# Kernel tuning notes

Measured on AMD Instinct MI355X. Metric: run time of the kernel, lower is better.

Reference implementation:

```python
import jax, jax.numpy as jnp
import numpy as np

B = 2; R_PER = 512; R = B * R_PER; RM_PER = 128; RM = B * RM_PER
NUM_CLASSES = 81; C = 256
IMG_H = 800.0; IMG_W = 800.0
SCALES = (0.25, 0.125, 0.0625, 0.03125)  # FPN strides 4,8,16,32
REG_W = (10.0, 10.0, 5.0, 5.0)
LOG_1000_16 = 4.135166556742356  # math.log(1000/16)


def _prep(c, size):
    # torchvision roi_align (aligned=False) coordinate handling
    valid = (c > -1.0) & (c < size)
    c = jnp.clip(c, 0.0, size - 1.0)
    lo = jnp.clip(jnp.floor(c), 0.0, size - 2.0).astype(jnp.int32)
    frac = c - lo.astype(c.dtype)
    return lo, frac, valid


def roi_align(feat, boxes, b_idx, scale, out_size, sr=2):
    # feat [B,C,H,W], boxes [R,4] in image coords, b_idx [R] int
    _, Cn, H, W = feat.shape
    bb = boxes * scale
    x1, y1 = bb[:, 0], bb[:, 1]
    rw = jnp.maximum(bb[:, 2] - x1, 1.0)
    rh = jnp.maximum(bb[:, 3] - y1, 1.0)
    n = out_size * sr
    g = (jnp.arange(n, dtype=feat.dtype) + 0.5) / (sr * out_size)
    ys = y1[:, None] + rh[:, None] * g[None, :]  # [R,n]
    xs = x1[:, None] + rw[:, None] * g[None, :]
    y0, ly, yv = _prep(ys, H)
    x0, lx, xv = _prep(xs, W)
    bi = b_idx[:, None, None]
    yy = y0[:, :, None]; xx = x0[:, None, :]
    f00 = feat[bi, :, yy, xx]          # [R,n,n,C]
    f01 = feat[bi, :, yy, xx + 1]
    f10 = feat[bi, :, yy + 1, xx]
    f11 = feat[bi, :, yy + 1, xx + 1]
    ly_ = ly[:, :, None, None]; lx_ = lx[:, None, :, None]
    v = (f00 * (1 - ly_) * (1 - lx_) + f01 * (1 - ly_) * lx_
         + f10 * ly_ * (1 - lx_) + f11 * ly_ * lx_)
    mask = (yv[:, :, None] & xv[:, None, :]).astype(v.dtype)[..., None]
    v = v * mask
    Rn = boxes.shape[0]
    v = v.reshape(Rn, out_size, sr, out_size, sr, Cn).mean(axis=(2, 4))
    return jnp.transpose(v, (0, 3, 1, 2))  # [R,C,out,out]


def multiscale_roi_align(feats, boxes, b_idx, out_size):
    area = jnp.maximum(boxes[:, 2] - boxes[:, 0], 0.0) * jnp.maximum(boxes[:, 3] - boxes[:, 1], 0.0)
    lvl = jnp.clip(jnp.floor(4.0 + jnp.log2(jnp.sqrt(area) / 224.0 + 1e-6)), 2.0, 5.0).astype(jnp.int32) - 2
    out = 0.0
    for i, (f, s) in enumerate(zip(feats, SCALES)):
        out = out + roi_align(f, boxes, b_idx, s, out_size) * (lvl == i)[:, None, None, None].astype(f.dtype)
    return out


def decode_boxes(deltas, boxes):
    # deltas [R,K,4], boxes [R,4]
    wx, wy, ww, wh = REG_W
    w = boxes[:, 2] - boxes[:, 0]; h = boxes[:, 3] - boxes[:, 1]
    cx = boxes[:, 0] + 0.5 * w; cy = boxes[:, 1] + 0.5 * h
    dx = deltas[..., 0] / wx; dy = deltas[..., 1] / wy
    dw = jnp.minimum(deltas[..., 2] / ww, LOG_1000_16)
    dh = jnp.minimum(deltas[..., 3] / wh, LOG_1000_16)
    pcx = dx * w[:, None] + cx[:, None]; pcy = dy * h[:, None] + cy[:, None]
    pw = jnp.exp(dw) * w[:, None]; ph = jnp.exp(dh) * h[:, None]
    out = jnp.stack([pcx - 0.5 * pw, pcy - 0.5 * ph, pcx + 0.5 * pw, pcy + 0.5 * ph], axis=-1)
    hi = jnp.array([IMG_W, IMG_H, IMG_W, IMG_H], dtype=out.dtype)
    return jnp.clip(out, 0.0, hi)  # process_box clip-to-image


def conv3x3(x, w, b):
    y = jax.lax.conv_general_dilated(x, w, (1, 1), ((1, 1), (1, 1)),
                                     dimension_numbers=('NCHW', 'OIHW', 'NCHW'))
    return jax.nn.relu(y + b[None, :, None, None])


def _forward(feat0, feat1, feat2, feat3, proposals, fc1_w, fc1_b, fc2_w, fc2_b,
             cls_w, cls_b, bbox_w, bbox_b, mconv_w, mconv_b, deconv_w, deconv_b,
             mlogit_w, mlogit_b, batch_idx):
    feats = (feat0, feat1, feat2, feat3)
    # box branch
    bf = multiscale_roi_align(feats, proposals, batch_idx, 7).reshape(R, -1)  # [R, 256*49]
    x = jax.nn.relu(bf @ fc1_w.T + fc1_b)
    x = jax.nn.relu(x @ fc2_w.T + fc2_b)
    scores = jax.nn.softmax(x @ cls_w.T + cls_b, axis=-1)          # [R,81]
    deltas = (x @ bbox_w.T + bbox_b).reshape(R, NUM_CLASSES, 4)
    boxes = decode_boxes(deltas, proposals)                        # [R,81,4]
    # mask branch on top-of-list detections (RM_PER per image), box at argmax fg class
    idx_m = jnp.concatenate([jnp.arange(RM_PER), R_PER + jnp.arange(RM_PER)])
    labels = jnp.argmax(scores[idx_m, 1:], axis=-1) + 1            # [RM]
    mboxes = boxes[idx_m, labels]                                  # [RM,4]
    mf = multiscale_roi_align(feats, mboxes, batch_idx[idx_m], 14)  # [RM,256,14,14]
    for i in range(4):
        mf = conv3x3(mf, mconv_w[i], mconv_b[i])
    # ConvTranspose2d k=2 s=2 (non-overlapping) as einsum, PyTorch IOHW weights
    t = jnp.einsum('bcij,copq->boipjq', mf, deconv_w).reshape(RM, C, 28, 28)
    t = jax.nn.relu(t + deconv_b[None, :, None, None])
    ml = jnp.einsum('bchw,oc->bohw', t, mlogit_w) + mlogit_b[None, :, None, None]
    masks = jax.nn.sigmoid(ml[jnp.arange(RM), labels])             # [RM,28,28]
    return scores, boxes, masks


def setup_inputs() -> dict:
    key = jax.random.key(0)
    ks = jax.random.split(key, 16)
    rn = lambda i, shape, s=1.0: jax.random.normal(ks[i], shape, dtype=jnp.float32) * s
    feat0 = rn(0, (B, C, 200, 200))
    feat1 = rn(1, (B, C, 100, 100))
    feat2 = rn(2, (B, C, 50, 50))
    feat3 = rn(3, (B, C, 25, 25))
    u = jax.random.uniform(ks[4], (R, 4), dtype=jnp.float32)
    x1 = u[:, 0] * (IMG_W - 64.0); y1 = u[:, 1] * (IMG_H - 64.0)
    w = 16.0 + u[:, 2] * 300.0; h = 16.0 + u[:, 3] * 300.0
    proposals = jnp.stack([x1, y1, jnp.minimum(x1 + w, IMG_W), jnp.minimum(y1 + h, IMG_H)], axis=1)
    batch_idx = jnp.repeat(jnp.arange(B, dtype=jnp.int32), R_PER)
    return dict(
        feat0=feat0, feat1=feat1, feat2=feat2, feat3=feat3,
        proposals=proposals,
        fc1_w=rn(5, (1024, C * 49), 0.01), fc1_b=jnp.zeros(1024, jnp.float32),
        fc2_w=rn(6, (1024, 1024), 0.02), fc2_b=jnp.zeros(1024, jnp.float32),
        cls_w=rn(7, (NUM_CLASSES, 1024), 0.02), cls_b=jnp.zeros(NUM_CLASSES, jnp.float32),
        bbox_w=rn(8, (NUM_CLASSES * 4, 1024), 0.01), bbox_b=jnp.zeros(NUM_CLASSES * 4, jnp.float32),
        mconv_w=rn(9, (4, C, C, 3, 3), 0.03), mconv_b=jnp.zeros((4, C), jnp.float32),
        deconv_w=rn(10, (C, C, 2, 2), 0.06), deconv_b=jnp.zeros(C, jnp.float32),
        mlogit_w=rn(11, (NUM_CLASSES, C), 0.06), mlogit_b=jnp.zeros(NUM_CLASSES, jnp.float32),
        batch_idx=batch_idx,
    )


def reference(feat0, feat1, feat2, feat3, proposals, fc1_w, fc1_b, fc2_w, fc2_b,
              cls_w, cls_b, bbox_w, bbox_b, mconv_w, mconv_b, deconv_w, deconv_b,
              mlogit_w, mlogit_b, batch_idx):
    return _forward(feat0, feat1, feat2, feat3, proposals, fc1_w, fc1_b, fc2_w, fc2_b,
                    cls_w, cls_b, bbox_w, bbox_b, mconv_w, mconv_b, deconv_w, deconv_b,
                    mlogit_w, mlogit_b, batch_idx)
```

## Files before the change

kernel.cpp:

```cpp
#include <hip/hip_runtime.h>


#define NUM_CLASSES 81
#define CDIM 256
#define RTOT 1024
#define RMASK 256
#define LOG1000_16 4.135166556742356f

typedef _Float16 half8v __attribute__((ext_vector_type(8)));
typedef _Float16 half4v __attribute__((ext_vector_type(4)));
typedef float    float4v __attribute__((ext_vector_type(4)));
typedef float    float2a4 __attribute__((ext_vector_type(2), aligned(4)));

__device__ __forceinline__ void gload_lds16(const void* g, void* l) {
    __builtin_amdgcn_global_load_lds(
        (const __attribute__((address_space(1))) void*)g,
        (__attribute__((address_space(3))) void*)l, 16, 0, 0);
}

__global__ __launch_bounds__(256) void roi_align7_kernel(
    const float* __restrict__ f0, const float* __restrict__ f1,
    const float* __restrict__ f2, const float* __restrict__ f3,
    const float* __restrict__ props, const int* __restrict__ bidx,
    _Float16* __restrict__ bf_h, _Float16* __restrict__ bf_l)
{
    int r  = blockIdx.x;
    int cg = blockIdx.y;
    int t = threadIdx.x;
    if (t >= 196) return;
    int p  = t % 49;
    int cl = t / 49;
    int oy = p / 7, ox = p % 7;

    float x1 = props[r*4+0], y1 = props[r*4+1];
    float x2 = props[r*4+2], y2 = props[r*4+3];
    float area = fmaxf(x2-x1, 0.f) * fmaxf(y2-y1, 0.f);
    float lf = floorf(4.f + log2f(sqrtf(area)/224.f + 1e-6f));
    lf = fminf(fmaxf(lf, 2.f), 5.f);
    int lvl = (int)lf - 2;

    const float* feat; int H, W; float scale;
    if (lvl == 0)      { feat = f0; H = 200; W = 200; scale = 0.25f; }
    else if (lvl == 1) { feat = f1; H = 100; W = 100; scale = 0.125f; }
    else if (lvl == 2) { feat = f2; H = 50;  W = 50;  scale = 0.0625f; }
    else               { feat = f3; H = 25;  W = 25;  scale = 0.03125f; }
    int b = bidx[r];

    float x1s = x1*scale, y1s = y1*scale;
    float rw = fmaxf(x2*scale - x1s, 1.f);
    float rh = fmaxf(y2*scale - y1s, 1.f);

    int   offs[4];
    float w00[4], w01[4], w10[4], w11[4];
    #pragma unroll
    for (int sy = 0; sy < 2; ++sy) {
        int iy = oy*2 + sy;
        float gy = ((float)iy + 0.5f) / 14.f;
        float yc = y1s + rh*gy;
        bool  yv = (yc > -1.f) && (yc < (float)H);
        float ycl = fminf(fmaxf(yc, 0.f), (float)(H-1));
        int   y0  = (int)fminf(floorf(ycl), (float)(H-2));
        float ly  = ycl - (float)y0;
        #pragma unroll
        for (int sx = 0; sx < 2; ++sx) {
            int ix = ox*2 + sx;
            float gx = ((float)ix + 0.5f) / 14.f;
            float xc = x1s + rw*gx;
            bool  xv = (xc > -1.f) && (xc < (float)W);
            float xcl = fminf(fmaxf(xc, 0.f), (float)(W-1));
            int   x0  = (int)fminf(floorf(xcl), (float)(W-2));
            float lx  = xcl - (float)x0;
            float m = (yv && xv) ? 1.f : 0.f;
            int s = sy*2 + sx;
            offs[s] = y0*W + x0;
            w00[s] = (1.f-ly)*(1.f-lx)*m;
            w01[s] = (1.f-ly)*lx*m;
            w10[s] = ly*(1.f-lx)*m;
            w11[s] = ly*lx*m;
        }
    }

    size_t HW = (size_t)H * W;
    #pragma unroll 4
    for (int k = 0; k < 16; ++k) {
        int c = cg*64 + cl + k*4;
        const float* fb = feat + ((size_t)b*CDIM + c) * HW;
        float acc = 0.f;
        #pragma unroll
        for (int s = 0; s < 4; ++s) {
            const float* q = fb + offs[s];
            float2a4 u = *(const float2a4*)q;
            float2a4 v = *(const float2a4*)(q + W);
            acc += w00[s]*u.x + w01[s]*u.y + w10[s]*v.x + w11[s]*v.y;
        }
        float v = acc * 0.25f;
        _Float16 h = (_Float16)v;
        size_t o = (size_t)r*12544 + c*49 + p;
        bf_h[o] = h;
        bf_l[o] = (_Float16)((v - (float)h) * 2048.f);
    }
}

template<bool BSPLIT>
__global__ __launch_bounds__(256, 2) void gemm_fc(
    const _Float16* __restrict__ Ah, const _Float16* __restrict__ Al,
    const float* __restrict__ B32,
    const _Float16* __restrict__ Bh16, const _Float16* __restrict__ Bl16,
    float* __restrict__ Cp, int K, int KS, int NS)
{
    __shared__ _Float16 AhL[2][128*32];
    __shared__ _Float16 AlL[2][128*32];
    __shared__ _Float16 BhL[2][64*32];
    __shared__ _Float16 BlL[2][64*32];

    int t = threadIdx.x;
    int lane = t & 63, wave = t >> 6;
    int wm = wave >> 1, wn = wave & 1;
    int ln = lane & 15, q = lane >> 4;

    int gx = gridDim.x, gy = gridDim.y;
    int lin = blockIdx.x + gx*(blockIdx.y + gy*blockIdx.z);
    int per = (gx*gy*(int)gridDim.z) >> 3;
    int nl  = (lin & 7)*per + (lin >> 3);
    int bn  = nl % gx;
    int tmp = nl / gx;
    int bm  = tmp % gy;
    int kz  = tmp / gy;

    int asub = lane >> 2;
    int achk = (lane & 3) ^ ((lane >> 3) & 3);
    int arow0 = (wave*2+0)*16 + asub;
    int arow1 = (wave*2+1)*16 + asub;
    const _Float16* Agh0 = Ah + (size_t)(bm*128+arow0)*K + (size_t)kz*KS + achk*8;
    const _Float16* Agh1 = Ah + (size_t)(bm*128+arow1)*K + (size_t)kz*KS + achk*8;
    const _Float16* Agl0 = Al + (size_t)(bm*128+arow0)*K + (size_t)kz*KS + achk*8;
    const _Float16* Agl1 = Al + (size_t)(bm*128+arow1)*K + (size_t)kz*KS + achk*8;
    int adst0 = (wave*2+0)*512;
    int adst1 = (wave*2+1)*512;

    const float*    Bs32 = nullptr;
    const _Float16 *Bgh = nullptr, *Bgl = nullptr;
    int bdst = 0, bwoff = 0;
    if constexpr (BSPLIT) {
        int brow = wave*16 + asub;
        Bgh = Bh16 + (size_t)(bn*64+brow)*K + (size_t)kz*KS + achk*8;
        Bgl = Bl16 + (size_t)(bn*64+brow)*K + (size_t)kz*KS + achk*8;
        bdst = wave*512;
    } else {
        int brow = t >> 2, bcp = t & 3;
        int bch = bcp ^ ((brow >> 1) & 3);
        Bs32 = B32 + (size_t)(bn*64+brow)*K + (size_t)kz*KS + bcp*8;
        bwoff = brow*32 + bch*8;
    }

    float4v acc1[4][2], acc2[4][2];
    #pragma unroll
    for (int i = 0; i < 4; ++i)
        #pragma unroll
        for (int j = 0; j < 2; ++j) {
            acc1[i][j] = (float4v){0.f,0.f,0.f,0.f};
            acc2[i][j] = (float4v){0.f,0.f,0.f,0.f};
        }

    int cq = (q ^ ((ln >> 1) & 3)) * 8;

    auto dma = [&](int k0, int nb) {
        gload_lds16(Agh0 + k0, &AhL[nb][adst0]);
        gload_lds16(Agh1 + k0, &AhL[nb][adst1]);
        gload_lds16(Agl0 + k0, &AlL[nb][adst0]);
        gload_lds16(Agl1 + k0, &AlL[nb][adst1]);
        if constexpr (BSPLIT) {
            gload_lds16(Bgh + k0, &BhL[nb][bdst]);
            gload_lds16(Bgl + k0, &BlL[nb][bdst]);
        }
    };
    auto bwrite = [&](const float4& v0, const float4& v1, int nb) {
        float vv[8] = {v0.x,v0.y,v0.z,v0.w,v1.x,v1.y,v1.z,v1.w};
        half8v h, l;
        #pragma unroll
        for (int j = 0; j < 8; ++j) {
            _Float16 hj = (_Float16)vv[j];
            h[j] = hj;
            l[j] = (_Float16)((vv[j] - (float)hj) * 2048.f);
        }
        *(half8v*)&BhL[nb][bwoff] = h;
        *(half8v*)&BlL[nb][bwoff] = l;
    };
    auto compute = [&](int pb) {
        half8v afh[4], afl[4], bfh[2], bfl[2];
        #pragma unroll
        for (int i = 0; i < 4; ++i) {
            int ra = (wm*64 + i*16 + ln)*32 + cq;
            afh[i] = *(const half8v*)&AhL[pb][ra];
            afl[i] = *(const half8v*)&AlL[pb][ra];
        }
        #pragma unroll
        for (int j = 0; j < 2; ++j) {
            int rb = (wn*32 + j*16 + ln)*32 + cq;
            bfh[j] = *(const half8v*)&BhL[pb][rb];
            bfl[j] = *(const half8v*)&BlL[pb][rb];
        }
        #pragma unroll
        for (int i = 0; i < 4; ++i) {
            #pragma unroll
            for (int j = 0; j < 2; ++j) {
                acc1[i][j] = __builtin_amdgcn_mfma_f32_16x16x32_f16(
                    afh[i], bfh[j], acc1[i][j], 0, 0, 0);
                acc2[i][j] = __builtin_amdgcn_mfma_f32_16x16x32_f16(
                    afh[i], bfl[j], acc2[i][j], 0, 0, 0);
                acc2[i][j] = __builtin_amdgcn_mfma_f32_16x16x32_f16(
                    afl[i], bfh[j], acc2[i][j], 0, 0, 0);
            }
        }
    };

    float4 bv0, bv1;
    if constexpr (!BSPLIT) {
        bv0 = *(const float4*)(Bs32);
        bv1 = *(const float4*)(Bs32 + 4);
    }
    dma(0, 0);
    if constexpr (!BSPLIT) bwrite(bv0, bv1, 0);
    __syncthreads();

    int pb = 0;
    for (int k0 = 32; k0 < KS; k0 += 32) {
        if constexpr (!BSPLIT) {
            bv0 = *(const float4*)(Bs32 + k0);
            bv1 = *(const float4*)(Bs32 + k0 + 4);
        }
        dma(k0, pb ^ 1);
        compute(pb);
        if constexpr (!BSPLIT) bwrite(bv0, bv1, pb ^ 1);
        __syncthreads();
        pb ^= 1;
    }
    compute(pb);

    float* Cpz = Cp + (size_t)kz*1024*NS;
    #pragma unroll
    for (int i = 0; i < 4; ++i) {
        #pragma unroll
        for (int j = 0; j < 2; ++j) {
            int col = bn*64 + wn*32 + j*16 + ln;
            #pragma unroll
            for (int reg = 0; reg < 4; ++reg) {
                int row = bm*128 + wm*64 + i*16 + q*4 + reg;
                Cpz[(size_t)row*NS + col] =
                    acc1[i][j][reg] + acc2[i][j][reg] * (1.f/2048.f);
            }
        }
    }
}

__global__ __launch_bounds__(256) void fc_reduce_kernel(
    const float* __restrict__ Cp, const float* __restrict__ bias,
    float* __restrict__ out, _Float16* __restrict__ outh,
    _Float16* __restrict__ outl, int nparts, int ns4, int do_relu)
{
    int i = blockIdx.x*256 + threadIdx.x;
    const float4* p = (const float4*)Cp;
    int pstride = 1024*ns4;
    float sx = 0.f, sy = 0.f, sz = 0.f, sw = 0.f;
    for (int j = 0; j < nparts; ++j) {
        float4 s = p[i + j*pstride];
        sx += s.x; sy += s.y; sz += s.z; sw += s.w;
    }
    float4 b4 = ((const float4*)bias)[i & (ns4-1)];
    float4 v;
    v.x = sx + b4.x; v.y = sy + b4.y; v.z = sz + b4.z; v.w = sw + b4.w;
    if (do_relu) {
        v.x = fmaxf(v.x, 0.f); v.y = fmaxf(v.y, 0.f);
        v.z = fmaxf(v.z, 0.f); v.w = fmaxf(v.w, 0.f);
    }
    if (out) ((float4*)out)[i] = v;
    if (outh) {
        float vv[4] = {v.x, v.y, v.z, v.w};
        half4v hh, hl;
        #pragma unroll
        for (int c2 = 0; c2 < 4; ++c2) {
            _Float16 h = (_Float16)vv[c2];
            hh[c2] = h;
            hl[c2] = (_Float16)((vv[c2] - (float)h) * 2048.f);
        }
        ((half4v*)outh)[i] = hh;
        ((half4v*)outl)[i] = hl;
    }
}

__global__ __launch_bounds__(256) void repack_head_kernel(
    const float* __restrict__ cls_w, const float* __restrict__ cls_b,
    const float* __restrict__ bbox_w, const float* __restrict__ bbox_b,
    _Float16* __restrict__ Wcat_h, _Float16* __restrict__ Wcat_l,
    float* __restrict__ bcat)
{
    int i = blockIdx.x*256 + threadIdx.x;
    int row = i >> 10, col = i & 1023;
    float v = 0.f;
    if (row < 81) v = cls_w[row*1024 + col];
    else if (row < 405) v = bbox_w[(row-81)*1024 + col];
    _Float16 h = (_Float16)v;
    Wcat_h[i] = h;
    Wcat_l[i] = (_Float16)((v - (float)h) * 2048.f);
    if (i < 512) {
        float bv = 0.f;
        if (i < 81) bv = cls_b[i];
        else if (i < 405) bv = bbox_b[i-81];
        bcat[i] = bv;
    }
}

__global__ __launch_bounds__(128) void heads_finish_kernel(
    const float* __restrict__ L, const float* __restrict__ props,
    float* __restrict__ scores, float* __restrict__ boxes,
    int* __restrict__ labels, float* __restrict__ mboxes)
{
    __shared__ float lg[NUM_CLASSES];
    __shared__ float red[2];
    __shared__ int slab;
    int r = blockIdx.x, t = threadIdx.x;
    const float* Lr = L + (size_t)r*512;
    if (t < NUM_CLASSES) lg[t] = Lr[t];
    __syncthreads();
    if (t == 0) {
        float mx = lg[0];
        for (int j = 1; j < NUM_CLASSES; ++j) mx = fmaxf(mx, lg[j]);
        red[0] = mx;
    }
    __syncthreads();
    float mx = red[0];
    if (t < NUM_CLASSES) lg[t] = expf(lg[t] - mx);
    __syncthreads();
    if (t == 0) {
        float s = 0.f;
        int best = 1; float bv = lg[1];
        for (int j = 0; j < NUM_CLASSES; ++j) {
            s += lg[j];
            if (j >= 1 && lg[j] > bv) { bv = lg[j]; best = j; }
        }
        red[1] = 1.f/s;
        slab = best;
    }
    __syncthreads();
    if (t < NUM_CLASSES) scores[(size_t)r*NUM_CLASSES + t] = lg[t]*red[1];

    bool sel = (r < 128) || (r >= 512 && r < 640);
    int mi = (r < 128) ? r : r - 384;
    if (t == 0 && sel) labels[mi] = slab;

    if (t < NUM_CLASSES) {
        float px1 = props[r*4+0], py1 = props[r*4+1];
        float px2 = props[r*4+2], py2 = props[r*4+3];
        float pw = px2 - px1, ph = py2 - py1;
        float cx = px1 + 0.5f*pw, cy = py1 + 0.5f*ph;
        const float* dl = Lr + 81 + t*4;
        float d0 = dl[0] * 0.1f;
        float d1 = dl[1] * 0.1f;
        float d2 = fminf(dl[2] * 0.2f, LOG1000_16);
        float d3 = fminf(dl[3] * 0.2f, LOG1000_16);
        float pcx = d0*pw + cx, pcy = d1*ph + cy;
        float qw = expf(d2)*pw, qh = expf(d3)*ph;
        float b0 = fminf(fmaxf(pcx - 0.5f*qw, 0.f), 800.f);
        float b1 = fminf(fmaxf(pcy - 0.5f*qh, 0.f), 800.f);
        float b2 = fminf(fmaxf(pcx + 0.5f*qw, 0.f), 800.f);
        float b3 = fminf(fmaxf(pcy + 0.5f*qh, 0.f), 800.f);
        size_t ob = ((size_t)r*NUM_CLASSES + t)*4;
        boxes[ob+0] = b0; boxes[ob+1] = b1; boxes[ob+2] = b2; boxes[ob+3] = b3;
        if (sel && t == slab) {
            mboxes[mi*4+0] = b0; mboxes[mi*4+1] = b1;
            mboxes[mi*4+2] = b2; mboxes[mi*4+3] = b3;
        }
    }
}

__global__ __launch_bounds__(256) void roi_align14_kernel(
    const float* __restrict__ f0, const float* __restrict__ f1,
    const float* __restrict__ f2, const float* __restrict__ f3,
    const float* __restrict__ mboxes, const int* __restrict__ bidx,
    _Float16* __restrict__ outT)
{
    int mi = blockIdx.x;
    int cg = blockIdx.y;
    int t = threadIdx.x;
    if (t >= 196) return;
    int oy = t / 14, ox = t % 14;

    float x1 = mboxes[mi*4+0], y1 = mboxes[mi*4+1];
    float x2 = mboxes[mi*4+2], y2 = mboxes[mi*4+3];
    float area = fmaxf(x2-x1, 0.f) * fmaxf(y2-y1, 0.f);
    float lf = floorf(4.f + log2f(sqrtf(area)/224.f + 1e-6f));
    lf = fminf(fmaxf(lf, 2.f), 5.f);
    int lvl = (int)lf - 2;

    const float* feat; int H, W; float scale;
    if (lvl == 0)      { feat = f0; H = 200; W = 200; scale = 0.25f; }
    else if (lvl == 1) { feat = f1; H = 100; W = 100; scale = 0.125f; }
    else if (lvl == 2) { feat = f2; H = 50;  W = 50;  scale = 0.0625f; }
    else               { feat = f3; H = 25;  W = 25;  scale = 0.03125f; }
    int ridx = (mi < 128) ? mi : mi + 384;
    int b = bidx[ridx];

    float x1s = x1*scale, y1s = y1*scale;
    float rw = fmaxf(x2*scale - x1s, 1.f);
    float rh = fmaxf(y2*scale - y1s, 1.f);

    int   offs[4];
    float w00[4], w01[4], w10[4], w11[4];
    #pragma unroll
    for (int sy = 0; sy < 2; ++sy) {
        int iy = oy*2 + sy;
        float gy = ((float)iy + 0.5f) / 28.f;
        float yc = y1s + rh*gy;
        bool  yv = (yc > -1.f) && (yc < (float)H);
        float ycl = fminf(fmaxf(yc, 0.f), (float)(H-1));
        int   y0  = (int)fminf(floorf(ycl), (float)(H-2));
        float ly  = ycl - (float)y0;
        #pragma unroll
        for (int sx = 0; sx < 2; ++sx) {
            int ix = ox*2 + sx;
            float gx = ((float)ix + 0.5f) / 28.f;
            float xc = x1s + rw*gx;
            bool  xv = (xc > -1.f) && (xc < (float)W);
            float xcl = fminf(fmaxf(xc, 0.f), (float)(W-1));
            int   x0  = (int)fminf(floorf(xcl), (float)(W-2));
            float lx  = xcl - (float)x0;
            float m = (yv && xv) ? 1.f : 0.f;
            int s = sy*2 + sx;
            offs[s] = y0*W + x0;
            w00[s] = (1.f-ly)*(1.f-lx)*m;
            w01[s] = (1.f-ly)*lx*m;
            w10[s] = ly*(1.f-lx)*m;
            w11[s] = ly*lx*m;
        }
    }

    size_t HW = (size_t)H * W;
    _Float16* orow = outT + ((size_t)mi*196 + t)*CDIM + cg*32;
    const float* fbase = feat + ((size_t)b*CDIM + cg*32) * HW;
    #pragma unroll
    for (int c8 = 0; c8 < 32; c8 += 8) {
        half8v hv;
        #pragma unroll
        for (int cc = 0; cc < 8; ++cc) {
            const float* fb = fbase + (size_t)(c8+cc) * HW;
            float acc = 0.f;
            #pragma unroll
            for (int s = 0; s < 4; ++s) {
                const float* q = fb + offs[s];
                float2a4 u = *(const float2a4*)q;
                float2a4 v = *(const float2a4*)(q + W);
                acc += w00[s]*u.x + w01[s]*u.y + w10[s]*v.x + w11[s]*v.y;
            }
            hv[cc] = (_Float16)(acc * 0.25f);
        }
        *(half8v*)(orow + c8) = hv;
    }
}

__global__ __launch_bounds__(256) void repack_wts_kernel(
    const float* __restrict__ w, _Float16* __restrict__ Wr)
{
    int i = blockIdx.x*256 + threadIdx.x;
    int ci = i & 255;
    int rest = i >> 8;
    int co = rest & 255;
    int rest2 = rest >> 8;
    int tap = rest2 % 9;
    int l = rest2 / 9;
    Wr[i] = (_Float16)w[(((size_t)(l*256 + co)*256 + ci)*9) + tap];
}

__global__ __launch_bounds__(256) void repack_dw_kernel(
    const float* __restrict__ dw, _Float16* __restrict__ Wd)
{
    int i = blockIdx.x*256 + threadIdx.x;
    int n = i >> 8, k = i & 255;
    Wd[i] = (_Float16)dw[(size_t)k*1024 + n];
}

#define PSTR 40

__global__ __launch_bounds__(256, 2) void conv3x3_mfma_kernel(
    const _Float16* __restrict__ inT, const _Float16* __restrict__ Wr,
    const float* __restrict__ bias, _Float16* __restrict__ outT, int layer)
{
    __shared__ _Float16 lin[256*PSTR];

    int t = threadIdx.x;
    int lane = t & 63;
    int wave = t >> 6;
    int ln = lane & 15;
    int q  = lane >> 4;
    int q8 = q*8;
    int r  = blockIdx.x >> 1;
    int bc = blockIdx.x & 1;
    int co_w = bc*128 + wave*32;

    const _Float16* WrL = Wr + (size_t)layer*9*256*256;
    const _Float16* inR = inT + (size_t)r*196*256;

    for (int i = t; i < 256*PSTR; i += 256) lin[i] = (_Float16)0.f;

    float4v acc[13][2];
    #pragma unroll
    for (int nt = 0; nt < 13; ++nt) {
        acc[nt][0] = (float4v){0.f,0.f,0.f,0.f};
        acc[nt][1] = (float4v){0.f,0.f,0.f,0.f};
    }

    for (int ci0 = 0; ci0 < 256; ci0 += 32) {
        __syncthreads();
        for (int idx = t; idx < 784; idx += 256) {
            int p = idx >> 2, g = idx & 3;
            float4 v = *(const float4*)(inR + (size_t)p*256 + ci0 + g*8);
            int row = (p*37450) >> 19;
            int col = p - row*14;
            *(float4*)&lin[((row+1)*16 + (col+1))*PSTR + g*8] = v;
        }
        __syncthreads();

        half8v aw[9][2];
        #pragma unroll
        for (int tap = 0; tap < 9; ++tap) {
            #pragma unroll
            for (int u = 0; u < 2; ++u)
                aw[tap][u] = *(const half8v*)(
                    WrL + ((size_t)tap*256 + co_w + u*16 + ln)*256 + ci0 + q8);
        }

        #pragma unroll
        for (int nt = 0; nt < 13; ++nt) {
            int n = nt*16 + ln;
            int row = (n*37450) >> 19;
            int col = n - row*14;
            int pb = (n < 196) ? (row*16 + col) : 0;
            const _Float16* bp = &lin[pb*PSTR + q8];
            #pragma unroll
            for (int ky = 0; ky < 3; ++ky) {
                #pragma unroll
                for (int kx = 0; kx < 3; ++kx) {
                    half8v bv = *(const half8v*)(bp + (ky*16 + kx)*PSTR);
                    acc[nt][0] = __builtin_amdgcn_mfma_f32_16x16x32_f16(
                        aw[ky*3+kx][0], bv, acc[nt][0], 0, 0, 0);
                    acc[nt][1] = __builtin_amdgcn_mfma_f32_16x16x32_f16(
                        aw[ky*3+kx][1], bv, acc[nt][1], 0, 0, 0);
                }
            }
        }
    }

    #pragma unroll
    for (int u = 0; u < 2; ++u) {
        float4 bi = *(const float4*)&bias[layer*256 + co_w + u*16 + q*4];
        float bia[4] = {bi.x, bi.y, bi.z, bi.w};
        #pragma unroll
        for (int nt = 0; nt < 13; ++nt) {
            int n = nt*16 + ln;
            if (n < 196) {
                half4v hv;
                #pragma unroll
                for (int i = 0; i < 4; ++i)
                    hv[i] = (_Float16)fmaxf(acc[nt][u][i] + bia[i], 0.f);
                *(half4v*)(outT + ((size_t)r*196 + n)*256 + co_w + u*16 + q*4) = hv;
            }
        }
    }
}

#define DSTR 264

template<int NMT>
__device__ __forceinline__ void deconv_pass(
    const _Float16* actL, const _Float16* __restrict__ Wd,
    const float* __restrict__ db, const float* __restrict__ mlw,
    int lab, float (*sred)[4], int wv, int ln, int q, int px0)
{
    float P[NMT][4];
    #pragma unroll
    for (int mt = 0; mt < NMT; ++mt)
        #pragma unroll
        for (int r2 = 0; r2 < 4; ++r2) P[mt][r2] = 0.f;

    for (int c = 0; c < 8; ++c) {
        int n0 = wv*256 + c*32;
        float4v acc[NMT][2];
        #pragma unroll
        for (int mt = 0; mt < NMT; ++mt) {
            acc[mt][0] = (float4v){0.f,0.f,0.f,0.f};
            acc[mt][1] = (float4v){0.f,0.f,0.f,0.f};
        }
        #pragma unroll
        for (int k = 0; k < 8; ++k) {
            const _Float16* wp = Wd + ((size_t)(n0 + ln))*256 + k*32 + q*8;
            half8v b0 = *(const half8v*)wp;
            half8v b1 = *(const half8v*)(wp + 16*256);
            #pragma unroll
            for (int mt = 0; mt < NMT; ++mt) {
                half8v a = *(const half8v*)&actL[(mt*16 + ln)*DSTR + k*32 + q*8];
                acc[mt][0] = __builtin_amdgcn_mfma_f32_16x16x32_f16(
                    a, b0, acc[mt][0], 0, 0, 0);
                acc[mt][1] = __builtin_amdgcn_mfma_f32_16x16x32_f16(
                    a, b1, acc[mt][1], 0, 0, 0);
            }
        }
        #pragma unroll
        for (int j = 0; j < 2; ++j) {
            int n = n0 + j*16 + ln;
            int o = n >> 2;
            float bo = db[o];
            float wl = mlw[lab*256 + o];
            #pragma unroll
            for (int mt = 0; mt < NMT; ++mt)
                #pragma unroll
                for (int r2 = 0; r2 < 4; ++r2)
                    P[mt][r2] += fmaxf(acc[mt][j][r2] + bo, 0.f) * wl;
        }
    }
    #pragma unroll
    for (int mt = 0; mt < NMT; ++mt)
        #pragma unroll
        for (int r2 = 0; r2 < 4; ++r2) {
            float v = P[mt][r2];
            v += __shfl_xor(v, 4);
            v += __shfl_xor(v, 8);
            int px = px0 + mt*16 + q*4 + r2;
            if (ln < 4 && px < 196) atomicAdd(&sred[px][ln], v);
        }
}

__global__ __launch_bounds__(256, 1) void deconv_mask_mfma_kernel(
    const _Float16* __restrict__ mfT, const _Float16* __restrict__ Wd,
    const float* __restrict__ db, const float* __restrict__ mlw,
    const float* __restrict__ mlb, const int* __restrict__ labels,
    float* __restrict__ masks)
{
    __shared__ _Float16 act[112*DSTR];
    __shared__ float sred[196][4];
    int t = threadIdx.x;
    int lane = t & 63, wv = t >> 6, ln = lane & 15, q = lane >> 4;
    int mi = blockIdx.x;
    int lab = labels[mi];

    for (int i = t; i < 784; i += 256) ((float*)sred)[i] = 0.f;

    for (int idx = t; idx < 112*32; idx += 256) {
        int px = idx >> 5, g = idx & 31;
        *(float4*)&act[px*DSTR + g*8] =
            *(const float4*)(mfT + ((size_t)mi*196 + px)*256 + g*8);
    }
    __syncthreads();
    deconv_pass<7>(act, Wd, db, mlw, lab, sred, wv, ln, q, 0);
    __syncthreads();

    for (int idx = t; idx < 84*32; idx += 256) {
        int px = idx >> 5, g = idx & 31;
        *(float4*)&act[px*DSTR + g*8] =
            *(const float4*)(mfT + ((size_t)mi*196 + 112 + px)*256 + g*8);
    }
    __syncthreads();
    deconv_pass<6>(act, Wd, db, mlw, lab, sred, wv, ln, q, 112);
    __syncthreads();

    if (t < 196) {
        float bl = mlb[lab];
        int i2 = t / 14, j2 = t % 14;
        #pragma unroll
        for (int pq = 0; pq < 4; ++pq) {
            float s = sred[t][pq] + bl;
            int h = 2*i2 + (pq >> 1), w2 = 2*j2 + (pq & 1);
            masks[(size_t)mi*784 + h*28 + w2] = 1.f/(1.f + expf(-s));
        }
    }
}

extern "C" void kernel_launch(void* const* d_in, const int* in_sizes, int n_in,
                              void* d_out, int out_size, void* d_ws, size_t ws_size,
                              hipStream_t stream) {
    const float* f0      = (const float*)d_in[0];
    const float* f1      = (const float*)d_in[1];
    const float* f2      = (const float*)d_in[2];
    const float* f3      = (const float*)d_in[3];
    const float* props   = (const float*)d_in[4];
    const float* fc1_w   = (const float*)d_in[5];
    const float* fc1_b   = (const float*)d_in[6];
    const float* fc2_w   = (const float*)d_in[7];
    const float* fc2_b   = (const float*)d_in[8];
    const float* cls_w   = (const float*)d_in[9];
    const float* cls_b   = (const float*)d_in[10];
    const float* bbox_w  = (const float*)d_in[11];
    const float* bbox_b  = (const float*)d_in[12];
    const float* mconv_w = (const float*)d_in[13];
    const float* mconv_b = (const float*)d_in[14];
    const float* dconv_w = (const float*)d_in[15];
    const float* dconv_b = (const float*)d_in[16];
    const float* mlog_w  = (const float*)d_in[17];
    const float* mlog_b  = (const float*)d_in[18];
    const int*   bidx    = (const int*)d_in[19];

    char* wsb = (char*)d_ws;
    _Float16* bf_h = (_Float16*)wsb;
    _Float16* bf_l = (_Float16*)(wsb + 25690112);
    _Float16* bufA = (_Float16*)wsb;
    _Float16* bufB = (_Float16*)(wsb + 25690112);
    _Float16* x1h  = (_Float16*)(wsb + 51380224);
    _Float16* x1l  = (_Float16*)(wsb + 53477376);
    _Float16* x2h  = (_Float16*)(wsb + 55574528);
    _Float16* x2l  = (_Float16*)(wsb + 57671680);
    int*      labels = (int*)(wsb + 59768832);
    float*    mboxes = (float*)(wsb + 59772928);
    float*    Cp     = (float*)(wsb + 59781120);
    _Float16* Wr     = (_Float16*)(wsb + 59781120);
    _Float16* Wd     = (_Float16*)(wsb + 64499712);
    _Float16* Wcat_h = (_Float16*)(wsb + 76558336);
    _Float16* Wcat_l = (_Float16*)(wsb + 77606912);
    float*    bcat   = (float*)(wsb + 78655488);
    float*    Lh     = (float*)(wsb + 78659584);

    float* scores = (float*)d_out;
    float* boxes  = scores + RTOT*NUM_CLASSES;
    float* masks  = boxes + RTOT*NUM_CLASSES*4;

    roi_align7_kernel<<<dim3(RTOT, 4), 256, 0, stream>>>(
        f0, f1, f2, f3, props, bidx, bf_h, bf_l);

    repack_head_kernel<<<2048, 256, 0, stream>>>(cls_w, cls_b, bbox_w, bbox_b,
                                                 Wcat_h, Wcat_l, bcat);

    gemm_fc<false><<<dim3(16, 8, 4), 256, 0, stream>>>(
        bf_h, bf_l, fc1_w, nullptr, nullptr, Cp, 12544, 3136, 1024);
    fc_reduce_kernel<<<1024, 256, 0, stream>>>(Cp, fc1_b, nullptr, x1h, x1l,
                                               4, 256, 1);

    gemm_fc<false><<<dim3(16, 8, 4), 256, 0, stream>>>(
        x1h, x1l, fc2_w, nullptr, nullptr, Cp, 1024, 256, 1024);
    fc_reduce_kernel<<<1024, 256, 0, stream>>>(Cp, fc2_b, nullptr, x2h, x2l,
                                               4, 256, 1);

    gemm_fc<true><<<dim3(8, 8, 4), 256, 0, stream>>>(
        x2h, x2l, nullptr, Wcat_h, Wcat_l, Cp, 1024, 256, 512);
    fc_reduce_kernel<<<512, 256, 0, stream>>>(Cp, bcat, Lh, nullptr, nullptr,
                                              4, 128, 0);

    heads_finish_kernel<<<RTOT, 128, 0, stream>>>(Lh, props, scores, boxes,
                                                  labels, mboxes);

    repack_wts_kernel<<<4*9*256, 256, 0, stream>>>(mconv_w, Wr);
    repack_dw_kernel<<<1024, 256, 0, stream>>>(dconv_w, Wd);

    roi_align14_kernel<<<dim3(RMASK, 8), 256, 0, stream>>>(
        f0, f1, f2, f3, mboxes, bidx, bufA);

    conv3x3_mfma_kernel<<<RMASK*2, 256, 0, stream>>>(bufA, Wr, mconv_b, bufB, 0);
    conv3x3_mfma_kernel<<<RMASK*2, 256, 0, stream>>>(bufB, Wr, mconv_b, bufA, 1);
    conv3x3_mfma_kernel<<<RMASK*2, 256, 0, stream>>>(bufA, Wr, mconv_b, bufB, 2);
    conv3x3_mfma_kernel<<<RMASK*2, 256, 0, stream>>>(bufB, Wr, mconv_b, bufA, 3);

    deconv_mask_mfma_kernel<<<RMASK, 256, 0, stream>>>(bufA, Wd, dconv_b, mlog_w,
                                                       mlog_b, labels, masks);
}
```

Measured before the change: 926.9 us.

## Rework FC GEMMs: 128x128 tiles, triple-buffered LDS DMA, fp32 B via LDS

Replaces the FC GEMM kernel with a 128x128 tile version that uses a three-stage LDS ring filled by async global-to-LDS loads, with vmcnt waits and a single barrier per k-step. For fc1, the fp32 weights are DMA'd into LDS with an XOR swizzle and split into fp16 hi/lo at fragment-load time, instead of being loaded into registers and written back to LDS. fc2 weights are pre-split by a new repack kernel, and the head GEMM uses split-K 8. The goal is to cut global traffic for the large fc1 weight and hide load latency, at the cost of occupancy one, 96KB of LDS and more conversion work in the inner loop.

```diff
diff --git a/kernel.cpp b/kernel.cpp
--- a/kernel.cpp
+++ b/kernel.cpp
@@ -101,17 +101,14 @@
     }
 }
 
-template<bool BSPLIT>
-__global__ __launch_bounds__(256, 2) void gemm_fc(
+template<int BMODE>
+__global__ __launch_bounds__(256, 1) void gemm_fc2(
     const _Float16* __restrict__ Ah, const _Float16* __restrict__ Al,
     const float* __restrict__ B32,
     const _Float16* __restrict__ Bh16, const _Float16* __restrict__ Bl16,
     float* __restrict__ Cp, int K, int KS, int NS)
 {
-    __shared__ _Float16 AhL[2][128*32];
-    __shared__ _Float16 AlL[2][128*32];
-    __shared__ _Float16 BhL[2][64*32];
-    __shared__ _Float16 BlL[2][64*32];
+    __shared__ __align__(16) char smem[3*32768];
 
     int t = threadIdx.x;
     int lane = t & 63, wave = t >> 6;
@@ -127,83 +124,114 @@
     int bm  = tmp % gy;
     int kz  = tmp / gy;
 
+    size_t kbase = (size_t)kz * KS;
     int asub = lane >> 2;
     int achk = (lane & 3) ^ ((lane >> 3) & 3);
-    int arow0 = (wave*2+0)*16 + asub;
-    int arow1 = (wave*2+1)*16 + asub;
-    const _Float16* Agh0 = Ah + (size_t)(bm*128+arow0)*K + (size_t)kz*KS + achk*8;
-    const _Float16* Agh1 = Ah + (size_t)(bm*128+arow1)*K + (size_t)kz*KS + achk*8;
-    const _Float16* Agl0 = Al + (size_t)(bm*128+arow0)*K + (size_t)kz*KS + achk*8;
-    const _Float16* Agl1 = Al + (size_t)(bm*128+arow1)*K + (size_t)kz*KS + achk*8;
-    int adst0 = (wave*2+0)*512;
-    int adst1 = (wave*2+1)*512;
-
-    const float*    Bs32 = nullptr;
-    const _Float16 *Bgh = nullptr, *Bgl = nullptr;
-    int bdst = 0, bwoff = 0;
-    if constexpr (BSPLIT) {
-        int brow = wave*16 + asub;
-        Bgh = Bh16 + (size_t)(bn*64+brow)*K + (size_t)kz*KS + achk*8;
-        Bgl = Bl16 + (size_t)(bn*64+brow)*K + (size_t)kz*KS + achk*8;
-        bdst = wave*512;
+
+    const _Float16* Agh0 = Ah + (size_t)(bm*128 + wave*32 + asub)*K + kbase + achk*8;
+    const _Float16* Agh1 = Agh0 + (size_t)16*K;
+    const _Float16* Agl0 = Al + (size_t)(bm*128 + wave*32 + asub)*K + kbase + achk*8;
+    const _Float16* Agl1 = Agl0 + (size_t)16*K;
+    int adst0 = (wave*32 + 0)*32;
+    int adst1 = (wave*32 + 16)*32;
+
+    const _Float16 *Bgh0=nullptr, *Bgh1=nullptr, *Bgl0=nullptr, *Bgl1=nullptr;
+    const float *Bg0=nullptr, *Bg1=nullptr, *Bg2=nullptr, *Bg3=nullptr;
+    int fdst0 = 0;
+    if constexpr (BMODE == 1) {
+        Bgh0 = Bh16 + (size_t)(bn*128 + wave*32 + asub)*K + kbase + achk*8;
+        Bgh1 = Bgh0 + (size_t)16*K;
+        Bgl0 = Bl16 + (size_t)(bn*128 + wave*32 + asub)*K + kbase + achk*8;
+        Bgl1 = Bgl0 + (size_t)16*K;
     } else {
-        int brow = t >> 2, bcp = t & 3;
-        int bch = bcp ^ ((brow >> 1) & 3);
-        Bs32 = B32 + (size_t)(bn*64+brow)*K + (size_t)kz*KS + bcp*8;
-        bwoff = brow*32 + bch*8;
-    }
-
-    float4v acc1[4][2], acc2[4][2];
+        int br8  = lane >> 3;
+        int bchk = (lane & 7) ^ br8;
+        const float* base = B32 + (size_t)(bn*128 + wave*32 + br8)*K + kbase + bchk*4;
+        Bg0 = base;
+        Bg1 = base + (size_t)8*K;
+        Bg2 = base + (size_t)16*K;
+        Bg3 = base + (size_t)24*K;
+        fdst0 = (wave*32)*32;
+    }
+
+    auto AhB = [&](int b){ return (_Float16*)(smem + b*32768); };
+    auto AlB = [&](int b){ return (_Float16*)(smem + b*32768 + 8192); };
+    auto BhB = [&](int b){ return (_Float16*)(smem + b*32768 + 16384); };
+    auto BlB = [&](int b){ return (_Float16*)(smem + b*32768 + 24576); };
+    auto BfB = [&](int b){ return (float*)   (smem + b*32768 + 16384); };
+
+    auto dma = [&](int k0, int b) {
+        gload_lds16(Agh0 + k0, AhB(b) + adst0);
+        gload_lds16(Agh1 + k0, AhB(b) + adst1);
+        gload_lds16(Agl0 + k0, AlB(b) + adst0);
+        gload_lds16(Agl1 + k0, AlB(b) + adst1);
+        if constexpr (BMODE == 1) {
+            gload_lds16(Bgh0 + k0, BhB(b) + adst0);
+            gload_lds16(Bgh1 + k0, BhB(b) + adst1);
+            gload_lds16(Bgl0 + k0, BlB(b) + adst0);
+            gload_lds16(Bgl1 + k0, BlB(b) + adst1);
+        } else {
+            gload_lds16(Bg0 + k0, BfB(b) + fdst0);
+            gload_lds16(Bg1 + k0, BfB(b) + fdst0 + 8*32);
+            gload_lds16(Bg2 + k0, BfB(b) + fdst0 + 16*32);
+            gload_lds16(Bg3 + k0, BfB(b) + fdst0 + 24*32);
+        }
+    };
+
+    float4v acc1[4][4], acc2[4][4];
     #pragma unroll
     for (int i = 0; i < 4; ++i)
         #pragma unroll
-        for (int j = 0; j < 2; ++j) {
+        for (int j = 0; j < 4; ++j) {
             acc1[i][j] = (float4v){0.f,0.f,0.f,0.f};
             acc2[i][j] = (float4v){0.f,0.f,0.f,0.f};
         }
 
     int cq = (q ^ ((ln >> 1) & 3)) * 8;
 
-    auto dma = [&](int k0, int nb) {
-        gload_lds16(Agh0 + k0, &AhL[nb][adst0]);
-        gload_lds16(Agh1 + k0, &AhL[nb][adst1]);
-        gload_lds16(Agl0 + k0, &AlL[nb][adst0]);
-        gload_lds16(Agl1 + k0, &AlL[nb][adst1]);
-        if constexpr (BSPLIT) {
-            gload_lds16(Bgh + k0, &BhL[nb][bdst]);
-            gload_lds16(Bgl + k0, &BlL[nb][bdst]);
-        }
-    };
-    auto bwrite = [&](const float4& v0, const float4& v1, int nb) {
-        float vv[8] = {v0.x,v0.y,v0.z,v0.w,v1.x,v1.y,v1.z,v1.w};
-        half8v h, l;
-        #pragma unroll
-        for (int j = 0; j < 8; ++j) {
-            _Float16 hj = (_Float16)vv[j];
-            h[j] = hj;
-            l[j] = (_Float16)((vv[j] - (float)hj) * 2048.f);
-        }
-        *(half8v*)&BhL[nb][bwoff] = h;
-        *(half8v*)&BlL[nb][bwoff] = l;
-    };
-    auto compute = [&](int pb) {
-        half8v afh[4], afl[4], bfh[2], bfl[2];
+    auto compute = [&](int b) {
+        const _Float16* ah = AhB(b);
+        const _Float16* al = AlB(b);
+        half8v afh[4], afl[4], bfh[4], bfl[4];
         #pragma unroll
         for (int i = 0; i < 4; ++i) {
             int ra = (wm*64 + i*16 + ln)*32 + cq;
-            afh[i] = *(const half8v*)&AhL[pb][ra];
-            afl[i] = *(const half8v*)&AlL[pb][ra];
-        }
-        #pragma unroll
-        for (int j = 0; j < 2; ++j) {
-            int rb = (wn*32 + j*16 + ln)*32 + cq;
-            bfh[j] = *(const half8v*)&BhL[pb][rb];
-            bfl[j] = *(const half8v*)&BlL[pb][rb];
+            afh[i] = *(const half8v*)&ah[ra];
+            afl[i] = *(const half8v*)&al[ra];
+        }
+        if constexpr (BMODE == 1) {
+            const _Float16* bh = BhB(b);
+            const _Float16* bl = BlB(b);
+            #pragma unroll
+            for (int j = 0; j < 4; ++j) {
+                int rb = (wn*64 + j*16 + ln)*32 + cq;
+                bfh[j] = *(const half8v*)&bh[rb];
+                bfl[j] = *(const half8v*)&bl[rb];
+            }
+        } else {
+            const float* bfp = BfB(b);
+            #pragma unroll
+            for (int j = 0; j < 4; ++j) {
+                int row = wn*64 + j*16 + ln;
+                int c0 = (q*2)   ^ (row & 7);
+                int c1 = (q*2+1) ^ (row & 7);
+                float4v f0 = *(const float4v*)&bfp[row*32 + c0*4];
+                float4v f1 = *(const float4v*)&bfp[row*32 + c1*4];
+                #pragma unroll
+                for (int e = 0; e < 4; ++e) {
+                    _Float16 h0 = (_Float16)f0[e];
+                    bfh[j][e] = h0;
+                    bfl[j][e] = (_Float16)((f0[e] - (float)h0) * 2048.f);
+                    _Float16 h1 = (_Float16)f1[e];
+                    bfh[j][4+e] = h1;
+                    bfl[j][4+e] = (_Float16)((f1[e] - (float)h1) * 2048.f);
+                }
+            }
         }
         #pragma unroll
         for (int i = 0; i < 4; ++i) {
             #pragma unroll
-            for (int j = 0; j < 2; ++j) {
+            for (int j = 0; j < 4; ++j) {
                 acc1[i][j] = __builtin_amdgcn_mfma_f32_16x16x32_f16(
                     afh[i], bfh[j], acc1[i][j], 0, 0, 0);
                 acc2[i][j] = __builtin_amdgcn_mfma_f32_16x16x32_f16(
@@ -214,35 +242,25 @@
         }
     };
 
-    float4 bv0, bv1;
-    if constexpr (!BSPLIT) {
-        bv0 = *(const float4*)(Bs32);
-        bv1 = *(const float4*)(Bs32 + 4);
-    }
+    int NT = KS / 32;
     dma(0, 0);
-    if constexpr (!BSPLIT) bwrite(bv0, bv1, 0);
-    __syncthreads();
-
-    int pb = 0;
-    for (int k0 = 32; k0 < KS; k0 += 32) {
-        if constexpr (!BSPLIT) {
-            bv0 = *(const float4*)(Bs32 + k0);
-            bv1 = *(const float4*)(Bs32 + k0 + 4);
-        }
-        dma(k0, pb ^ 1);
-        compute(pb);
-        if constexpr (!BSPLIT) bwrite(bv0, bv1, pb ^ 1);
-        __syncthreads();
-        pb ^= 1;
-    }
-    compute(pb);
+    if (NT > 1) dma(32, 1);
+
+    for (int tt = 0; tt < NT; ++tt) {
+        if (tt < NT-1) asm volatile("s_waitcnt vmcnt(8)" ::: "memory");
+        else           asm volatile("s_waitcnt vmcnt(0)" ::: "memory");
+        __builtin_amdgcn_s_barrier();
+        asm volatile("" ::: "memory");
+        if (tt + 2 < NT) dma((tt+2)*32, (tt+2)%3);
+        compute(tt%3);
+    }
 
     float* Cpz = Cp + (size_t)kz*1024*NS;
     #pragma unroll
     for (int i = 0; i < 4; ++i) {
         #pragma unroll
-        for (int j = 0; j < 2; ++j) {
-            int col = bn*64 + wn*32 + j*16 + ln;
+        for (int j = 0; j < 4; ++j) {
+            int col = bn*128 + wn*64 + j*16 + ln;
             #pragma unroll
             for (int reg = 0; reg < 4; ++reg) {
                 int row = bm*128 + wm*64 + i*16 + q*4 + reg;
@@ -286,6 +304,24 @@
         ((half4v*)outh)[i] = hh;
         ((half4v*)outl)[i] = hl;
     }
+}
+
+__global__ __launch_bounds__(256) void repack_split_kernel(
+    const float* __restrict__ w, _Float16* __restrict__ h,
+    _Float16* __restrict__ l)
+{
+    int i = blockIdx.x*256 + threadIdx.x;
+    float4 v = ((const float4*)w)[i];
+    float vv[4] = {v.x, v.y, v.z, v.w};
+    half4v hh, hl;
+    #pragma unroll
+    for (int c2 = 0; c2 < 4; ++c2) {
+        _Float16 hj = (_Float16)vv[c2];
+        hh[c2] = hj;
+        hl[c2] = (_Float16)((vv[c2] - (float)hj) * 2048.f);
+    }
+    ((half4v*)h)[i] = hh;
+    ((half4v*)l)[i] = hl;
 }
 
 __global__ __launch_bounds__(256) void repack_head_kernel(
@@ -700,6 +736,8 @@
     char* wsb = (char*)d_ws;
     _Float16* bf_h = (_Float16*)wsb;
     _Float16* bf_l = (_Float16*)(wsb + 25690112);
+    _Float16* fc2h = (_Float16*)wsb;
+    _Float16* fc2l = (_Float16*)(wsb + 2097152);
     _Float16* bufA = (_Float16*)wsb;
     _Float16* bufB = (_Float16*)(wsb + 25690112);
     _Float16* x1h  = (_Float16*)(wsb + 51380224);
@@ -726,20 +764,22 @@
     repack_head_kernel<<<2048, 256, 0, stream>>>(cls_w, cls_b, bbox_w, bbox_b,
                                                  Wcat_h, Wcat_l, bcat);
 
-    gemm_fc<false><<<dim3(16, 8, 4), 256, 0, stream>>>(
+    gemm_fc2<0><<<dim3(8, 8, 4), 256, 0, stream>>>(
         bf_h, bf_l, fc1_w, nullptr, nullptr, Cp, 12544, 3136, 1024);
     fc_reduce_kernel<<<1024, 256, 0, stream>>>(Cp, fc1_b, nullptr, x1h, x1l,
                                                4, 256, 1);
 
-    gemm_fc<false><<<dim3(16, 8, 4), 256, 0, stream>>>(
-        x1h, x1l, fc2_w, nullptr, nullptr, Cp, 1024, 256, 1024);
+    repack_split_kernel<<<1024, 256, 0, stream>>>(fc2_w, fc2h, fc2l);
+
+    gemm_fc2<1><<<dim3(8, 8, 4), 256, 0, stream>>>(
+        x1h, x1l, nullptr, fc2h, fc2l, Cp, 1024, 256, 1024);
     fc_reduce_kernel<<<1024, 256, 0, stream>>>(Cp, fc2_b, nullptr, x2h, x2l,
                                                4, 256, 1);
 
-    gemm_fc<true><<<dim3(8, 8, 4), 256, 0, stream>>>(
-        x2h, x2l, nullptr, Wcat_h, Wcat_l, Cp, 1024, 256, 512);
+    gemm_fc2<1><<<dim3(4, 8, 8), 256, 0, stream>>>(
+        x2h, x2l, nullptr, Wcat_h, Wcat_l, Cp, 1024, 128, 512);
     fc_reduce_kernel<<<512, 256, 0, stream>>>(Cp, bcat, Lh, nullptr, nullptr,
-                                              4, 128, 0);
+                                              8, 128, 0);
 
     heads_finish_kernel<<<RTOT, 128, 0, stream>>>(Lh, props, scores, boxes,
                                                   labels, mboxes);
```

Measured after the change: 882.0 us. 1.05x faster.
